# Kernel optimization log

Hardware: AMD Instinct MI355X
Metric: run time of the kernel (lower is better)

## Reference

```python
import jax, jax.numpy as jnp
import numpy as np

N, CIN, H, W = 4, 64, 160, 256
INS_PER = 16
T = N * INS_PER            # total instances = sum(num_ins)
CH, OUT = 16, 1
WN = [(CIN + 2) * CH, CH * CH, CH * OUT]   # [1056, 256, 16]
BN = [CH, CH, OUT]
P = sum(WN) + sum(BN)      # 1361
MASK_BIAS_SHIFT = 2.19


def setup_inputs() -> dict:
    key = jax.random.key(0)
    k1, k2 = jax.random.split(key)
    x = jax.random.normal(k1, (N, CIN, H, W), dtype=jnp.float32)
    mask_head_params = jax.random.normal(k2, (T, P), dtype=jnp.float32) * 0.1
    num_ins = jnp.full((N,), INS_PER, dtype=jnp.int32)
    return {"x": x, "mask_head_params": mask_head_params, "num_ins": num_ins}


def reference(x, mask_head_params, num_ins):
    n, c, h, w = x.shape
    # compute_locations with stride=1: locations = stack((shift_x, shift_y)) + 0
    # NOTE: the original `locations[:0] /= H` / `locations[:1] /= W` are
    # zero-size slices (no-ops), so coords remain unnormalized.
    ys, xs = jnp.meshgrid(jnp.arange(h, dtype=jnp.float32),
                          jnp.arange(w, dtype=jnp.float32), indexing='ij')
    loc = jnp.stack([xs, ys], axis=0)                       # [2, H, W]
    loc = jnp.broadcast_to(loc[None], (n, 2, h, w))
    xc = jnp.concatenate([loc, x], axis=1)                  # [N, C+2, H, W]

    # per-image repeat -> one feature copy per instance
    feat = jnp.repeat(xc, num_ins, axis=0, total_repeat_length=T)  # [T, C+2, H, W]

    # parse dynamic params (mask=True: last bias shifted by -2.19)
    p = mask_head_params
    o = 0
    w0 = p[:, o:o + WN[0]].reshape(T, CH, CIN + 2); o += WN[0]
    w1 = p[:, o:o + WN[1]].reshape(T, CH, CH);      o += WN[1]
    w2 = p[:, o:o + WN[2]].reshape(T, OUT, CH);     o += WN[2]
    b0 = p[:, o:o + BN[0]]; o += BN[0]
    b1 = p[:, o:o + BN[1]]; o += BN[1]
    b2 = p[:, o:o + BN[2]] - MASK_BIAS_SHIFT

    # grouped 1x1 convs (groups=num_insts) == per-instance linear over HxW
    hdn = jax.nn.relu(jnp.einsum('toi,tihw->tohw', w0, feat) + b0[:, :, None, None])
    hdn = jax.nn.relu(jnp.einsum('toi,tihw->tohw', w1, hdn) + b1[:, :, None, None])
    out = jnp.einsum('toi,tihw->tohw', w2, hdn) + b2[:, :, None, None]
    return out.reshape(1, T * OUT, h, w)
```

## Files before the change

### kernel.cpp

```cpp
#include <hip/hip_runtime.h>


#define CIN  64
#define HH   160
#define WW   256
#define HWSZ (HH * WW)
#define PP   1361
#define MASK_BIAS_SHIFT 2.19f
#define PKF  1280
#define NSPLIT 2
#define NT   5
#define MAXI 8
#define BLKPX (16 * NT * 4)

typedef short short8 __attribute__((ext_vector_type(8)));
typedef float f32x4  __attribute__((ext_vector_type(4)));

union BF8 { short8 s; __bf16 b[8]; };

__device__ inline __bf16 bhi(float v) { return (__bf16)v; }
__device__ inline __bf16 blo(float v) { return (__bf16)(v - (float)(__bf16)v); }


__global__ __launch_bounds__(64) void prep_params(
    const float* __restrict__ params, float* __restrict__ pk)
{
    const int t    = blockIdx.x;
    const int lane = threadIdx.x;
    const int col  = lane & 15;
    const int g    = lane >> 4;
    const float* pw = params + (size_t)t * PP;
    float* dst = pk + (size_t)t * PKF;

    const __bf16 z = (__bf16)0.f;

    BF8 a00, a01;
#pragma unroll
    for (int j = 0; j < 8; ++j) {
        a00.b[j] = (__bf16)pw[col * 66 + 2 +      g * 8 + j];
        a01.b[j] = (__bf16)pw[col * 66 + 2 + 32 + g * 8 + j];
    }

    BF8 a1b;
#pragma unroll
    for (int j = 0; j < 4; ++j)
        a1b.b[j] = (__bf16)pw[1056 + col * 16 + g * 4 + j];
    {
        const float b1 = pw[1344 + col];
        a1b.b[4] = (g == 0) ? bhi(b1) : z;
        a1b.b[5] = (g == 0) ? blo(b1) : z;
        a1b.b[6] = z;  a1b.b[7] = z;
    }

    BF8 a2r;
#pragma unroll
    for (int j = 0; j < 4; ++j) a2r.b[j] = (__bf16)pw[1312 + g * 4 + j];
    {
        const float b2 = pw[1360] - MASK_BIAS_SHIFT;
        a2r.b[4] = (g == 0) ? bhi(b2) : z;
        a2r.b[5] = (g == 0) ? blo(b2) : z;
        a2r.b[6] = z;  a2r.b[7] = z;
    }

    BF8 ca;
    {
        const float wx = pw[col * 66 + 0];
        const float wy = pw[col * 66 + 1];
        const float b0 = pw[1328 + col];
        ca.b[0] = (g == 0) ? bhi(wx) : z;
        ca.b[1] = (g == 0) ? blo(wx) : z;
        ca.b[2] = (g == 0) ? bhi(wy) : z;
        ca.b[3] = (g == 0) ? blo(wy) : z;
        ca.b[4] = (g == 0) ? bhi(b0) : z;
        ca.b[5] = (g == 0) ? blo(b0) : z;
        ca.b[6] = z; ca.b[7] = z;
    }

    ((short8*)(dst       ))[lane] = a00.s;
    ((short8*)(dst +  256))[lane] = a01.s;
    ((short8*)(dst +  512))[lane] = a1b.s;
    ((short8*)(dst +  768))[lane] = a2r.s;
    ((short8*)(dst + 1024))[lane] = ca.s;
}

__global__ __launch_bounds__(256, 4) void mask_head_v12(
    const float* __restrict__ x,
    const float* __restrict__ pk,
    const int*   __restrict__ num_ins,
    float*       __restrict__ out,
    int N, int T)
{
    __shared__ __align__(16) float plds[MAXI][PKF];

    const int tid  = threadIdx.x;
    const int wave = tid >> 6;
    const int lane = tid & 63;
    const int col  = lane & 15;
    const int g    = lane >> 4;
    const int n    = blockIdx.y;
    const int s    = blockIdx.z;
    const int pxw  = blockIdx.x * BLKPX + wave * (16 * NT);

    int t0 = 0;
    for (int j = 0; j < n; ++j) t0 += num_ins[j];
    int t1 = t0 + num_ins[n];
    if (n == N - 1) t1 = T;
    if (t1 > T) t1 = T;
    t0 = __builtin_amdgcn_readfirstlane(t0);
    t1 = __builtin_amdgcn_readfirstlane(t1);
    const int M = t1 - t0;

    int mloc = (M - s + NSPLIT - 1) / NSPLIT;
    if (mloc < 0) mloc = 0;
    if (mloc > MAXI) mloc = MAXI;

    for (int c = tid; c < mloc * (PKF / 4); c += 256) {
        const int i   = c / (PKF / 4);
        const int off = c - i * (PKF / 4);
        const int t   = t0 + s + NSPLIT * i;
        ((f32x4*)plds[i])[off] = ((const f32x4*)(pk + (size_t)t * PKF))[off];
    }
    __syncthreads();

    BF8 xb[NT][2];
    const float* xbase = x + (size_t)n * CIN * HWSZ + pxw + col;
#pragma unroll
    for (int nt = 0; nt < NT; ++nt)
#pragma unroll
        for (int c = 0; c < 2; ++c)
#pragma unroll
            for (int j = 0; j < 8; ++j) {
                const int ch = c * 32 + g * 8 + j;
                xb[nt][c].b[j] = (__bf16)xbase[(size_t)ch * HWSZ + nt * 16];
            }

    BF8 b2c[NT];
#pragma unroll
    for (int nt = 0; nt < NT; ++nt) {
        const int px = pxw + nt * 16 + col;
        const __bf16 xfb = (__bf16)(float)(px & (WW - 1));
        const __bf16 yfb = (__bf16)(float)(px >> 8);
        b2c[nt].b[0] = xfb; b2c[nt].b[1] = xfb;
        b2c[nt].b[2] = yfb; b2c[nt].b[3] = yfb;
        b2c[nt].b[4] = (__bf16)1.f; b2c[nt].b[5] = (__bf16)1.f;
        b2c[nt].b[6] = (__bf16)0.f; b2c[nt].b[7] = (__bf16)0.f;
    }

    const __bf16 one = (__bf16)1.f, zero = (__bf16)0.f;

    for (int i = 0; i < mloc; ++i) {
        const int t = t0 + s + NSPLIT * i;
        const short8* fp = (const short8*)plds[i];

        short8 ca  = fp[256 + lane];
        short8 a00 = fp[       lane];
        short8 a01 = fp[ 64 + lane];

        f32x4 acc[NT];
#pragma unroll
        for (int nt = 0; nt < NT; ++nt) {
            f32x4 z4 = {0.f, 0.f, 0.f, 0.f};
            acc[nt] = __builtin_amdgcn_mfma_f32_16x16x32_bf16(ca, b2c[nt].s, z4, 0, 0, 0);
        }
#pragma unroll
        for (int nt = 0; nt < NT; ++nt)
            acc[nt] = __builtin_amdgcn_mfma_f32_16x16x32_bf16(a00, xb[nt][0].s, acc[nt], 0, 0, 0);
#pragma unroll
        for (int nt = 0; nt < NT; ++nt)
            acc[nt] = __builtin_amdgcn_mfma_f32_16x16x32_bf16(a01, xb[nt][1].s, acc[nt], 0, 0, 0);

        BF8 h[NT];
#pragma unroll
        for (int nt = 0; nt < NT; ++nt) {
#pragma unroll
            for (int j = 0; j < 4; ++j) h[nt].b[j] = (__bf16)fmaxf(acc[nt][j], 0.f);
            h[nt].b[4] = one; h[nt].b[5] = one; h[nt].b[6] = zero; h[nt].b[7] = zero;
        }

        short8 a1b = fp[128 + lane];
#pragma unroll
        for (int nt = 0; nt < NT; ++nt) {
            f32x4 z4 = {0.f, 0.f, 0.f, 0.f};
            acc[nt] = __builtin_amdgcn_mfma_f32_16x16x32_bf16(a1b, h[nt].s, z4, 0, 0, 0);
        }

#pragma unroll
        for (int nt = 0; nt < NT; ++nt) {
#pragma unroll
            for (int j = 0; j < 4; ++j) h[nt].b[j] = (__bf16)fmaxf(acc[nt][j], 0.f);
            h[nt].b[4] = one; h[nt].b[5] = one; h[nt].b[6] = zero; h[nt].b[7] = zero;
        }

        short8 a2r = fp[192 + lane];
#pragma unroll
        for (int nt = 0; nt < NT; ++nt) {
            f32x4 z4 = {0.f, 0.f, 0.f, 0.f};
            acc[nt] = __builtin_amdgcn_mfma_f32_16x16x32_bf16(a2r, h[nt].s, z4, 0, 0, 0);
        }

        float oval = 0.f, t4 = 0.f;
#pragma unroll
        for (int nt = 0; nt < NT; ++nt) {
            if (nt == g)  oval = acc[nt][0];
            if (nt == 4)  t4   = acc[nt][0];
        }
        float* const op = out + (size_t)t * HWSZ + pxw;
        op[lane] = oval;
        if (g == 0) op[64 + col] = t4;
    }
}

__global__ __launch_bounds__(256) void mask_head_mfma_nows(
    const float* __restrict__ x,
    const float* __restrict__ params,
    const int*   __restrict__ num_ins,
    float*       __restrict__ out,
    int N, int T)
{
    const int tid  = threadIdx.x;
    const int wave = tid >> 6;
    const int lane = tid & 63;
    const int col  = lane & 15;
    const int g    = lane >> 4;
    const int n    = blockIdx.y;
    const int pxw  = blockIdx.x * 256 + wave * 64;

    int t0 = 0;
    for (int j = 0; j < n; ++j) t0 += num_ins[j];
    int t1 = t0 + num_ins[n];
    if (n == N - 1) t1 = T;
    if (t1 > T) t1 = T;

    BF8 xb[4][2];
    const float* xbase = x + (size_t)n * CIN * HWSZ + pxw + col;
#pragma unroll
    for (int nt = 0; nt < 4; ++nt)
#pragma unroll
        for (int c = 0; c < 2; ++c)
#pragma unroll
            for (int j = 0; j < 8; ++j)
                xb[nt][c].b[j] = (__bf16)xbase[(size_t)(c * 32 + g * 8 + j) * HWSZ + nt * 16];

    float xf[4], yf[4];
#pragma unroll
    for (int nt = 0; nt < 4; ++nt) {
        const int pix = pxw + nt * 16 + col;
        xf[nt] = (float)(pix & (WW - 1));
        yf[nt] = (float)(pix >> 8);
    }

    for (int t = t0; t < t1; ++t) {
        const float* pw = params + (size_t)t * PP;
        BF8 a00, a01, a1;
#pragma unroll
        for (int j = 0; j < 8; ++j) {
            a00.b[j] = (__bf16)pw[col * 66 + 2 +      g * 8 + j];
            a01.b[j] = (__bf16)pw[col * 66 + 2 + 32 + g * 8 + j];
        }
#pragma unroll
        for (int j = 0; j < 4; ++j) {
            a1.b[j]     = (__bf16)pw[1056 + col * 16 + g * 4 + j];
            a1.b[4 + j] = (__bf16)0.f;
        }
        float wxv[4], wyv[4], b0v[4], b1v[4], w2v[4];
#pragma unroll
        for (int j = 0; j < 4; ++j) {
            const int r = g * 4 + j;
            wxv[j] = pw[r * 66 + 0];
            wyv[j] = pw[r * 66 + 1];
            b0v[j] = pw[1328 + r];
            b1v[j] = pw[1344 + r];
            w2v[j] = pw[1312 + r];
        }
        const float b2v = pw[1360] - MASK_BIAS_SHIFT;

        f32x4 acc0[4];
#pragma unroll
        for (int nt = 0; nt < 4; ++nt) {
            f32x4 a = {0.f, 0.f, 0.f, 0.f};
            a = __builtin_amdgcn_mfma_f32_16x16x32_bf16(a00.s, xb[nt][0].s, a, 0, 0, 0);
            a = __builtin_amdgcn_mfma_f32_16x16x32_bf16(a01.s, xb[nt][1].s, a, 0, 0, 0);
            acc0[nt] = a;
        }
        BF8 h0[4];
#pragma unroll
        for (int nt = 0; nt < 4; ++nt)
#pragma unroll
            for (int j = 0; j < 4; ++j) {
                float v = acc0[nt][j] + b0v[j];
                v = fmaf(wxv[j], xf[nt], v);
                v = fmaf(wyv[j], yf[nt], v);
                v = fmaxf(v, 0.f);
                h0[nt].b[j]     = (__bf16)v;
                h0[nt].b[4 + j] = (__bf16)0.f;
            }
        f32x4 acc1[4];
#pragma unroll
        for (int nt = 0; nt < 4; ++nt) {
            f32x4 a = {0.f, 0.f, 0.f, 0.f};
            acc1[nt] = __builtin_amdgcn_mfma_f32_16x16x32_bf16(a1.s, h0[nt].s, a, 0, 0, 0);
        }
        float oval = 0.f;
#pragma unroll
        for (int nt = 0; nt < 4; ++nt) {
            float sum = 0.f;
#pragma unroll
            for (int j = 0; j < 4; ++j) {
                const float h = fmaxf(acc1[nt][j] + b1v[j], 0.f);
                sum = fmaf(w2v[j], h, sum);
            }
            sum += __shfl_xor(sum, 16, 64);
            sum += __shfl_xor(sum, 32, 64);
            if (nt == g) oval = sum + b2v;
        }
        out[(size_t)t * HWSZ + pxw + lane] = oval;
    }
}

extern "C" void kernel_launch(void* const* d_in, const int* in_sizes, int n_in,
                              void* d_out, int out_size, void* d_ws, size_t ws_size,
                              hipStream_t stream) {
    const float* x      = (const float*)d_in[0];
    const float* params = (const float*)d_in[1];
    const int*   nins   = (const int*)d_in[2];
    float*       out    = (float*)d_out;

    const int N = in_sizes[2];
    const int T = in_sizes[1] / PP;
    const size_t ws_needed = (size_t)T * PKF * sizeof(float);

    if (ws_size >= ws_needed) {
        float* pk = (float*)d_ws;
        prep_params<<<T, dim3(64), 0, stream>>>(params, pk);
        dim3 grid(HWSZ / BLKPX, N, NSPLIT);
        mask_head_v12<<<grid, dim3(256), 0, stream>>>(x, pk, nins, out, N, T);
    } else {
        dim3 grid(HWSZ / 256, N);
        mask_head_mfma_nows<<<grid, dim3(256), 0, stream>>>(x, params, nins, out, N, T);
    }
}
```

Before: 31.25 us.

## Pre-transpose input to pixel-major bf16 in prep kernel and vector-load in main kernel

```diff
diff --git a/kernel.cpp b/kernel.cpp
--- a/kernel.cpp
+++ b/kernel.cpp
@@ -12,6 +12,8 @@
 #define NT   5
 #define MAXI 8
 #define BLKPX (16 * NT * 4)
+#define XT_OFF 524288
+#define PXCHUNKS (HWSZ / 64)
 
 typedef short short8 __attribute__((ext_vector_type(8)));
 typedef float f32x4  __attribute__((ext_vector_type(4)));
@@ -22,69 +24,110 @@
 __device__ inline __bf16 blo(float v) { return (__bf16)(v - (float)(__bf16)v); }
 
 
-__global__ __launch_bounds__(64) void prep_params(
-    const float* __restrict__ params, float* __restrict__ pk)
+__global__ __launch_bounds__(256) void prep_all(
+    const float* __restrict__ x,
+    const float* __restrict__ params,
+    float*       __restrict__ pk,
+    short*       __restrict__ xt,
+    int N, int T, int ntrb)
 {
-    const int t    = blockIdx.x;
-    const int lane = threadIdx.x;
-    const int col  = lane & 15;
-    const int g    = lane >> 4;
-    const float* pw = params + (size_t)t * PP;
-    float* dst = pk + (size_t)t * PKF;
-
-    const __bf16 z = (__bf16)0.f;
-
-    BF8 a00, a01;
-#pragma unroll
-    for (int j = 0; j < 8; ++j) {
-        a00.b[j] = (__bf16)pw[col * 66 + 2 +      g * 8 + j];
-        a01.b[j] = (__bf16)pw[col * 66 + 2 + 32 + g * 8 + j];
-    }
-
-    BF8 a1b;
-#pragma unroll
-    for (int j = 0; j < 4; ++j)
-        a1b.b[j] = (__bf16)pw[1056 + col * 16 + g * 4 + j];
+    const int tid = threadIdx.x;
+
+    if ((int)blockIdx.x >= ntrb) {
+        const int t = (blockIdx.x - ntrb) * 4 + (tid >> 6);
+        if (t >= T) return;
+        const int lane = tid & 63;
+        const int col  = lane & 15;
+        const int g    = lane >> 4;
+        const float* pw = params + (size_t)t * PP;
+        float* dst = pk + (size_t)t * PKF;
+        const __bf16 z = (__bf16)0.f;
+
+        BF8 a00, a01;
+#pragma unroll
+        for (int j = 0; j < 8; ++j) {
+            a00.b[j] = (__bf16)pw[col * 66 + 2 +      g * 8 + j];
+            a01.b[j] = (__bf16)pw[col * 66 + 2 + 32 + g * 8 + j];
+        }
+
+        BF8 a1b;
+#pragma unroll
+        for (int j = 0; j < 4; ++j)
+            a1b.b[j] = (__bf16)pw[1056 + col * 16 + g * 4 + j];
+        {
+            const float b1 = pw[1344 + col];
+            a1b.b[4] = (g == 0) ? bhi(b1) : z;
+            a1b.b[5] = (g == 0) ? blo(b1) : z;
+            a1b.b[6] = z;  a1b.b[7] = z;
+        }
+
+        BF8 a2r;
+#pragma unroll
+        for (int j = 0; j < 4; ++j) a2r.b[j] = (__bf16)pw[1312 + g * 4 + j];
+        {
+            const float b2 = pw[1360] - MASK_BIAS_SHIFT;
+            a2r.b[4] = (g == 0) ? bhi(b2) : z;
+            a2r.b[5] = (g == 0) ? blo(b2) : z;
+            a2r.b[6] = z;  a2r.b[7] = z;
+        }
+
+        BF8 ca;
+        {
+            const float wx = pw[col * 66 + 0];
+            const float wy = pw[col * 66 + 1];
+            const float b0 = pw[1328 + col];
+            ca.b[0] = (g == 0) ? bhi(wx) : z;
+            ca.b[1] = (g == 0) ? blo(wx) : z;
+            ca.b[2] = (g == 0) ? bhi(wy) : z;
+            ca.b[3] = (g == 0) ? blo(wy) : z;
+            ca.b[4] = (g == 0) ? bhi(b0) : z;
+            ca.b[5] = (g == 0) ? blo(b0) : z;
+            ca.b[6] = z; ca.b[7] = z;
+        }
+
+        ((short8*)(dst       ))[lane] = a00.s;
+        ((short8*)(dst +  256))[lane] = a01.s;
+        ((short8*)(dst +  512))[lane] = a1b.s;
+        ((short8*)(dst +  768))[lane] = a2r.s;
+        ((short8*)(dst + 1024))[lane] = ca.s;
+        return;
+    }
+
+    __shared__ float tile[CIN][65];
+    const int n   = blockIdx.x / PXCHUNKS;
+    const int px0 = (blockIdx.x % PXCHUNKS) * 64;
+    const float* src = x + (size_t)n * CIN * HWSZ + px0;
+
+#pragma unroll
+    for (int k = 0; k < 4; ++k) {
+        const int idx = k * 256 + tid;
+        const int ch  = idx >> 4;
+        const int f4  = idx & 15;
+        const f32x4 v = *(const f32x4*)(src + (size_t)ch * HWSZ + f4 * 4);
+        tile[ch][f4 * 4 + 0] = v[0];
+        tile[ch][f4 * 4 + 1] = v[1];
+        tile[ch][f4 * 4 + 2] = v[2];
+        tile[ch][f4 * 4 + 3] = v[3];
+    }
+    __syncthreads();
+
     {
-        const float b1 = pw[1344 + col];
-        a1b.b[4] = (g == 0) ? bhi(b1) : z;
-        a1b.b[5] = (g == 0) ? blo(b1) : z;
-        a1b.b[6] = z;  a1b.b[7] = z;
-    }
-
-    BF8 a2r;
-#pragma unroll
-    for (int j = 0; j < 4; ++j) a2r.b[j] = (__bf16)pw[1312 + g * 4 + j];
-    {
-        const float b2 = pw[1360] - MASK_BIAS_SHIFT;
-        a2r.b[4] = (g == 0) ? bhi(b2) : z;
-        a2r.b[5] = (g == 0) ? blo(b2) : z;
-        a2r.b[6] = z;  a2r.b[7] = z;
-    }
-
-    BF8 ca;
-    {
-        const float wx = pw[col * 66 + 0];
-        const float wy = pw[col * 66 + 1];
-        const float b0 = pw[1328 + col];
-        ca.b[0] = (g == 0) ? bhi(wx) : z;
-        ca.b[1] = (g == 0) ? blo(wx) : z;
-        ca.b[2] = (g == 0) ? bhi(wy) : z;
-        ca.b[3] = (g == 0) ? blo(wy) : z;
-        ca.b[4] = (g == 0) ? bhi(b0) : z;
-        ca.b[5] = (g == 0) ? blo(b0) : z;
-        ca.b[6] = z; ca.b[7] = z;
-    }
-
-    ((short8*)(dst       ))[lane] = a00.s;
-    ((short8*)(dst +  256))[lane] = a01.s;
-    ((short8*)(dst +  512))[lane] = a1b.s;
-    ((short8*)(dst +  768))[lane] = a2r.s;
-    ((short8*)(dst + 1024))[lane] = ca.s;
+        const int px = tid >> 2;
+        const int q  = tid & 3;
+        BF8 lo, hi;
+#pragma unroll
+        for (int i = 0; i < 8; ++i) {
+            lo.b[i] = (__bf16)tile[q * 16 + i    ][px];
+            hi.b[i] = (__bf16)tile[q * 16 + i + 8][px];
+        }
+        short* dst = xt + ((size_t)n * HWSZ + px0 + px) * CIN + q * 16;
+        *(short8*)(dst    ) = lo.s;
+        *(short8*)(dst + 8) = hi.s;
+    }
 }
 
-__global__ __launch_bounds__(256, 4) void mask_head_v12(
-    const float* __restrict__ x,
+__global__ __launch_bounds__(256, 4) void mask_head_v13(
+    const short* __restrict__ xt,
     const float* __restrict__ pk,
     const int*   __restrict__ num_ins,
     float*       __restrict__ out,
@@ -120,19 +163,14 @@
         const int t   = t0 + s + NSPLIT * i;
         ((f32x4*)plds[i])[off] = ((const f32x4*)(pk + (size_t)t * PKF))[off];
     }
-    __syncthreads();
 
     BF8 xb[NT][2];
-    const float* xbase = x + (size_t)n * CIN * HWSZ + pxw + col;
+    const short* xtp = xt + ((size_t)n * HWSZ + pxw) * CIN;
 #pragma unroll
     for (int nt = 0; nt < NT; ++nt)
 #pragma unroll
         for (int c = 0; c < 2; ++c)
-#pragma unroll
-            for (int j = 0; j < 8; ++j) {
-                const int ch = c * 32 + g * 8 + j;
-                xb[nt][c].b[j] = (__bf16)xbase[(size_t)ch * HWSZ + nt * 16];
-            }
+            xb[nt][c].s = *(const short8*)(xtp + (nt * 16 + col) * CIN + c * 32 + g * 8);
 
     BF8 b2c[NT];
 #pragma unroll
@@ -147,6 +185,7 @@
     }
 
     const __bf16 one = (__bf16)1.f, zero = (__bf16)0.f;
+    __syncthreads();
 
     for (int i = 0; i < mloc; ++i) {
         const int t = t0 + s + NSPLIT * i;
@@ -327,13 +366,16 @@
 
     const int N = in_sizes[2];
     const int T = in_sizes[1] / PP;
-    const size_t ws_needed = (size_t)T * PKF * sizeof(float);
+    const int ntrb = N * PXCHUNKS;
+    const size_t ws_needed = (size_t)XT_OFF + (size_t)N * HWSZ * CIN * 2;
 
     if (ws_size >= ws_needed) {
         float* pk = (float*)d_ws;
-        prep_params<<<T, dim3(64), 0, stream>>>(params, pk);
+        short* xt = (short*)((char*)d_ws + XT_OFF);
+        prep_all<<<ntrb + (T + 3) / 4, dim3(256), 0, stream>>>(
+            x, params, pk, xt, N, T, ntrb);
         dim3 grid(HWSZ / BLKPX, N, NSPLIT);
-        mask_head_v12<<<grid, dim3(256), 0, stream>>>(x, pk, nins, out, N, T);
+        mask_head_v13<<<grid, dim3(256), 0, stream>>>(xt, pk, nins, out, N, T);
     } else {
         dim3 grid(HWSZ / 256, N);
         mask_head_mfma_nows<<<grid, dim3(256), 0, stream>>>(x, params, nins, out, N, T);
```

Measured after the change: 35.77 us. 14.5% more time.
